# Kernel optimization log

Measured on AMD Instinct MI355X. Metric: run time of the kernel, lower is better.

The kernel has to match this reference:

```python
import jax, jax.numpy as jnp
import numpy as np


def setup_inputs() -> dict:
    key = jax.random.key(0)
    kq, kk, kv, km = jax.random.split(key, 4)
    B, H, S, D = 2, 16, 2048, 64
    Q = jax.random.normal(kq, (B, H, S, D), dtype=jnp.float32)
    K = jax.random.normal(kk, (B, H, S, D), dtype=jnp.float32)
    V = jax.random.normal(kv, (B, H, S, D), dtype=jnp.float32)
    attn_mask = jax.random.randint(km, (B, 1, S, S), 0, 2, dtype=jnp.int32)
    return {"Q": Q, "K": K, "V": V, "attn_mask": attn_mask}


def reference(Q, K, V, attn_mask):
    d_k = jnp.asarray(K.shape[-1], dtype=Q.dtype)
    # scores: [B,H,S,S]
    scores = jnp.einsum("bhqd,bhkd->bhqk", Q, K) / jnp.sqrt(d_k)
    scores = jnp.where(attn_mask == 0, jnp.asarray(-1e9, scores.dtype), scores)
    attn_weights = jax.nn.softmax(scores, axis=-1)
    context = jnp.einsum("bhqk,bhkd->bhqd", attn_weights, V)
    return context, attn_weights
```

## Files before the change

### kernel.cpp

```cpp
#include <hip/hip_runtime.h>
#include <hip/hip_bf16.h>

typedef __attribute__((ext_vector_type(8))) short      short8;
typedef __attribute__((ext_vector_type(4))) float      floatx4;

#define DI __device__ __forceinline__

constexpr int BB = 2, HH = 16, SS = 2048, DD = 64;
constexpr int TQ  = 64;
constexpr int TK  = 64;
constexpr int NKT = SS / TK;
constexpr int PITCH = 72;

DI unsigned short f2bfu(float f) {
    __hip_bfloat16 h = __float2bfloat16(f);
    return __builtin_bit_cast(unsigned short, h);
}

DI short8 cvt8(const float* __restrict__ p) {
    floatx4 a = *(const floatx4*)p;
    floatx4 b = *(const floatx4*)(p + 4);
    short8 r;
    r[0] = (short)f2bfu(a[0]); r[1] = (short)f2bfu(a[1]);
    r[2] = (short)f2bfu(a[2]); r[3] = (short)f2bfu(a[3]);
    r[4] = (short)f2bfu(b[0]); r[5] = (short)f2bfu(b[1]);
    r[6] = (short)f2bfu(b[2]); r[7] = (short)f2bfu(b[3]);
    return r;
}

__global__ __launch_bounds__(256, 2)
void sdpa_kernel(const float* __restrict__ Q,
                 const float* __restrict__ K,
                 const float* __restrict__ V,
                 const int*   __restrict__ mask,
                 float*       __restrict__ out_ctx,
                 float*       __restrict__ out_w)
{
    __shared__ __align__(16) unsigned short Vt[DD * PITCH];
    __shared__ __align__(16) unsigned short Pl[TQ * PITCH];

    const int tid  = (int)threadIdx.x;
    const int wave = tid >> 6;
    const int lane = tid & 63;
    const int quad = lane >> 4;
    const int col  = lane & 15;

    const int bh = (int)blockIdx.y;
    const int b  = bh >> 4;
    const int q0 = (int)blockIdx.x * TQ;
    const int qw = q0 + wave * 16;

    const size_t head = (size_t)bh * SS * DD;
    const float* Qh = Q + head;
    const float* Kh = K + head;
    const float* Vh = V + head;
    const int*   Mb = mask  + (size_t)b  * SS * SS;
    float*       Wh = out_w + (size_t)bh * SS * SS;

    short8 aQ0, aQ1;
    {
        const float* qp = Qh + (size_t)(qw + col) * DD + quad * 8;
        aQ0 = cvt8(qp);
        aQ1 = cvt8(qp + 32);
    }

    float mrow[4], lrow[4];
#pragma unroll
    for (int r = 0; r < 4; ++r) { mrow[r] = -__builtin_inff(); lrow[r] = 0.f; }

    for (int kt = 0; kt < NKT; ++kt) {
        const int kv0 = kt * TK;
        floatx4 acc[4];
#pragma unroll
        for (int nt = 0; nt < 4; ++nt) {
            const float* kp = Kh + (size_t)(kv0 + nt * 16 + col) * DD + quad * 8;
            short8 b0 = cvt8(kp);
            short8 b1 = cvt8(kp + 32);
            floatx4 a = {0.f, 0.f, 0.f, 0.f};
            a = __builtin_amdgcn_mfma_f32_16x16x32_bf16(aQ0, b0, a, 0, 0, 0);
            a = __builtin_amdgcn_mfma_f32_16x16x32_bf16(aQ1, b1, a, 0, 0, 0);
            acc[nt] = a;
        }
#pragma unroll
        for (int r = 0; r < 4; ++r) {
            const int q = qw + quad * 4 + r;
            const int* mp = Mb + (size_t)q * SS + kv0 + col;
            float s0 = acc[0][r] * 0.125f; s0 = (mp[0]  != 0) ? s0 : -1e9f;
            float s1 = acc[1][r] * 0.125f; s1 = (mp[16] != 0) ? s1 : -1e9f;
            float s2 = acc[2][r] * 0.125f; s2 = (mp[32] != 0) ? s2 : -1e9f;
            float s3 = acc[3][r] * 0.125f; s3 = (mp[48] != 0) ? s3 : -1e9f;
            float lm = fmaxf(fmaxf(s0, s1), fmaxf(s2, s3));
            float mn = fmaxf(mrow[r], lm);
            float p  = __expf(s0 - mn) + __expf(s1 - mn) + __expf(s2 - mn) + __expf(s3 - mn);
            lrow[r]  = lrow[r] * __expf(mrow[r] - mn) + p;
            mrow[r]  = mn;
        }
    }
#pragma unroll
    for (int r = 0; r < 4; ++r) {
#pragma unroll
        for (int off = 1; off < 16; off <<= 1) {
            float mo = __shfl_xor(mrow[r], off);
            float lo = __shfl_xor(lrow[r], off);
            float mn = fmaxf(mrow[r], mo);
            lrow[r] = lrow[r] * __expf(mrow[r] - mn) + lo * __expf(mo - mn);
            mrow[r] = mn;
        }
    }
    float rl[4];
#pragma unroll
    for (int r = 0; r < 4; ++r) rl[r] = 1.0f / lrow[r];

    floatx4 ctx[4];
#pragma unroll
    for (int nt = 0; nt < 4; ++nt) ctx[nt] = floatx4{0.f, 0.f, 0.f, 0.f};

    for (int kt = 0; kt < NKT; ++kt) {
        const int kv0 = kt * TK;

        floatx4 acc[4];
#pragma unroll
        for (int nt = 0; nt < 4; ++nt) {
            const float* kp = Kh + (size_t)(kv0 + nt * 16 + col) * DD + quad * 8;
            short8 b0 = cvt8(kp);
            short8 b1 = cvt8(kp + 32);
            floatx4 a = {0.f, 0.f, 0.f, 0.f};
            a = __builtin_amdgcn_mfma_f32_16x16x32_bf16(aQ0, b0, a, 0, 0, 0);
            a = __builtin_amdgcn_mfma_f32_16x16x32_bf16(aQ1, b1, a, 0, 0, 0);
            acc[nt] = a;
        }

        __syncthreads();

        {
            const int kvr = tid >> 2;
            const int d0  = (tid & 3) * 16;
            const float* vp = Vh + (size_t)(kv0 + kvr) * DD + d0;
            floatx4 v0 = *(const floatx4*)vp;
            floatx4 v1 = *(const floatx4*)(vp + 4);
            floatx4 v2 = *(const floatx4*)(vp + 8);
            floatx4 v3 = *(const floatx4*)(vp + 12);
#pragma unroll
            for (int i = 0; i < 4; ++i) Vt[(d0 + i)      * PITCH + kvr] = f2bfu(v0[i]);
#pragma unroll
            for (int i = 0; i < 4; ++i) Vt[(d0 + 4 + i)  * PITCH + kvr] = f2bfu(v1[i]);
#pragma unroll
            for (int i = 0; i < 4; ++i) Vt[(d0 + 8 + i)  * PITCH + kvr] = f2bfu(v2[i]);
#pragma unroll
            for (int i = 0; i < 4; ++i) Vt[(d0 + 12 + i) * PITCH + kvr] = f2bfu(v3[i]);
        }

#pragma unroll
        for (int r = 0; r < 4; ++r) {
            const int q = qw + quad * 4 + r;
            const int* mp = Mb + (size_t)q * SS + kv0 + col;
            float* wp = Wh + (size_t)q * SS + kv0 + col;
#pragma unroll
            for (int nt = 0; nt < 4; ++nt) {
                float v = acc[nt][r] * 0.125f;
                v = (mp[nt * 16] != 0) ? v : -1e9f;
                float w = __expf(v - mrow[r]) * rl[r];
                wp[nt * 16] = w;
                Pl[(wave * 16 + quad * 4 + r) * PITCH + nt * 16 + col] = f2bfu(w);
            }
        }

        __syncthreads();

        short8 pA0 = *(const short8*)&Pl[(wave * 16 + col) * PITCH + quad * 8];
        short8 pA1 = *(const short8*)&Pl[(wave * 16 + col) * PITCH + 32 + quad * 8];
#pragma unroll
        for (int nt = 0; nt < 4; ++nt) {
            short8 vB0 = *(const short8*)&Vt[(nt * 16 + col) * PITCH + quad * 8];
            short8 vB1 = *(const short8*)&Vt[(nt * 16 + col) * PITCH + 32 + quad * 8];
            ctx[nt] = __builtin_amdgcn_mfma_f32_16x16x32_bf16(pA0, vB0, ctx[nt], 0, 0, 0);
            ctx[nt] = __builtin_amdgcn_mfma_f32_16x16x32_bf16(pA1, vB1, ctx[nt], 0, 0, 0);
        }
    }

#pragma unroll
    for (int nt = 0; nt < 4; ++nt) {
#pragma unroll
        for (int r = 0; r < 4; ++r) {
            const int q = qw + quad * 4 + r;
            out_ctx[head + (size_t)q * DD + nt * 16 + col] = ctx[nt][r];
        }
    }
}

extern "C" void kernel_launch(void* const* d_in, const int* in_sizes, int n_in,
                              void* d_out, int out_size, void* d_ws, size_t ws_size,
                              hipStream_t stream) {
    const float* Q = (const float*)d_in[0];
    const float* K = (const float*)d_in[1];
    const float* V = (const float*)d_in[2];
    const int* mask = (const int*)d_in[3];

    float* out     = (float*)d_out;
    float* out_ctx = out;
    float* out_w   = out + (size_t)BB * HH * SS * DD;

    dim3 grid(SS / TQ, BB * HH);
    hipLaunchKernelGGL(sdpa_kernel, grid, dim3(256), 0, stream,
                       Q, K, V, mask, out_ctx, out_w);
}
```

Before: 1.051 ms.

## Precompute bf16 K, transposed V and bitpacked mask in a prep kernel

Adds a prep kernel that converts K to bf16, writes V transposed in bf16 to workspace, and packs the int32 mask into 64-bit ballot words. The main kernel becomes one 64-thread wave per 16 query rows. It reads the preconverted operands directly, folds the 1/sqrt(d) scale into Q, and stages probabilities in LDS so attention weights go out as coalesced nontemporal vector stores. This removes repeated per-block fp32 to bf16 conversion and the heavy int32 mask reads in both passes, at the cost of an extra launch, workspace traffic, and smaller blocks with more global V loads.

New measurement: 889.2 us. 1.18x faster.

```diff
diff --git a/kernel.cpp b/kernel.cpp
--- a/kernel.cpp
+++ b/kernel.cpp
@@ -3,23 +3,27 @@
 
 typedef __attribute__((ext_vector_type(8))) short      short8;
 typedef __attribute__((ext_vector_type(4))) float      floatx4;
+typedef unsigned long long u64;
+typedef unsigned short     u16;
 
 #define DI __device__ __forceinline__
 
 constexpr int BB = 2, HH = 16, SS = 2048, DD = 64;
-constexpr int TQ  = 64;
 constexpr int TK  = 64;
 constexpr int NKT = SS / TK;
-constexpr int PITCH = 72;
-
-DI unsigned short f2bfu(float f) {
+constexpr int PW  = 68;
+
+constexpr size_t NELEM  = (size_t)BB * HH * SS * DD;
+constexpr size_t OFF_VT = NELEM * 2;
+constexpr size_t OFF_MB = OFF_VT + NELEM * 2;
+constexpr size_t NWORDS = (size_t)BB * SS * (SS / 64);
+
+DI u16 f2bfu(float f) {
     __hip_bfloat16 h = __float2bfloat16(f);
-    return __builtin_bit_cast(unsigned short, h);
-}
-
-DI short8 cvt8(const float* __restrict__ p) {
-    floatx4 a = *(const floatx4*)p;
-    floatx4 b = *(const floatx4*)(p + 4);
+    return __builtin_bit_cast(u16, h);
+}
+
+DI short8 pack8(floatx4 a, floatx4 b) {
     short8 r;
     r[0] = (short)f2bfu(a[0]); r[1] = (short)f2bfu(a[1]);
     r[2] = (short)f2bfu(a[2]); r[3] = (short)f2bfu(a[3]);
@@ -28,40 +32,99 @@
     return r;
 }
 
-__global__ __launch_bounds__(256, 2)
-void sdpa_kernel(const float* __restrict__ Q,
-                 const float* __restrict__ K,
-                 const float* __restrict__ V,
-                 const int*   __restrict__ mask,
-                 float*       __restrict__ out_ctx,
-                 float*       __restrict__ out_w)
+DI short8 cvt8s(const float* __restrict__ p, float s) {
+    floatx4 a = *(const floatx4*)p;
+    floatx4 b = *(const floatx4*)(p + 4);
+    a *= s; b *= s;
+    return pack8(a, b);
+}
+
+constexpr int KBLK = 2048;
+constexpr int VBLK = 1024;
+constexpr int MBLK = 4096;
+
+__global__ __launch_bounds__(256)
+void prep_kernel(const float* __restrict__ K, const float* __restrict__ V,
+                 const int* __restrict__ mask,
+                 u16* __restrict__ Kb, u16* __restrict__ Vt, u64* __restrict__ Mb)
 {
-    __shared__ __align__(16) unsigned short Vt[DD * PITCH];
-    __shared__ __align__(16) unsigned short Pl[TQ * PITCH];
-
-    const int tid  = (int)threadIdx.x;
-    const int wave = tid >> 6;
-    const int lane = tid & 63;
+    const int bx = (int)blockIdx.x, tid = (int)threadIdx.x;
+    if (bx < KBLK) {
+        size_t i = ((size_t)bx * 256 + tid) * 8;
+        floatx4 a = *(const floatx4*)(K + i);
+        floatx4 b = *(const floatx4*)(K + i + 4);
+        *(short8*)(Kb + i) = pack8(a, b);
+    } else if (bx < KBLK + VBLK) {
+        __shared__ __align__(16) u16 T[DD * 72];
+        const int idx = bx - KBLK;
+        const int bh = idx >> 5, kt = idx & 31;
+        const int kvr = tid >> 2, d0 = (tid & 3) * 16;
+        const float* vp = V + ((size_t)bh * SS + kt * 64 + kvr) * DD + d0;
+        floatx4 v0 = *(const floatx4*)vp;
+        floatx4 v1 = *(const floatx4*)(vp + 4);
+        floatx4 v2 = *(const floatx4*)(vp + 8);
+        floatx4 v3 = *(const floatx4*)(vp + 12);
+#pragma unroll
+        for (int i = 0; i < 4; ++i) T[(d0 + i)      * 72 + kvr] = f2bfu(v0[i]);
+#pragma unroll
+        for (int i = 0; i < 4; ++i) T[(d0 + 4 + i)  * 72 + kvr] = f2bfu(v1[i]);
+#pragma unroll
+        for (int i = 0; i < 4; ++i) T[(d0 + 8 + i)  * 72 + kvr] = f2bfu(v2[i]);
+#pragma unroll
+        for (int i = 0; i < 4; ++i) T[(d0 + 12 + i) * 72 + kvr] = f2bfu(v3[i]);
+        __syncthreads();
+        const int d = tid >> 2, seg = (tid & 3) * 16;
+        short8 s0 = *(const short8*)&T[d * 72 + seg];
+        short8 s1 = *(const short8*)&T[d * 72 + seg + 8];
+        u16* op = Vt + ((size_t)bh * DD + d) * SS + kt * 64 + seg;
+        *(short8*)op       = s0;
+        *(short8*)(op + 8) = s1;
+    } else {
+        const int mc = bx - (KBLK + VBLK);
+        const int wv = tid >> 6, lane = tid & 63;
+        const size_t gw = (size_t)mc * 4 + wv;
+#pragma unroll
+        for (int it = 0; it < 8; ++it) {
+            size_t word = gw * 8 + it;
+            int b   = (int)(word >> 16);
+            int rem = (int)(word & 65535);
+            int q = rem >> 5, wj = rem & 31;
+            int v = mask[((size_t)b * SS + q) * SS + wj * 64 + lane];
+            u64 bal = __ballot(v != 0);
+            if (lane == 0) Mb[word] = bal;
+        }
+    }
+}
+
+__global__ __launch_bounds__(64, 4)
+void sdpa_main(const float* __restrict__ Q,
+               const u16*   __restrict__ Kb,
+               const u16*   __restrict__ Vt,
+               const u64*   __restrict__ Mb,
+               float*       __restrict__ out_ctx,
+               float*       __restrict__ out_w)
+{
+    __shared__ __align__(16) float Pw[16 * PW];
+
+    const int lane = (int)threadIdx.x;
     const int quad = lane >> 4;
     const int col  = lane & 15;
 
     const int bh = (int)blockIdx.y;
     const int b  = bh >> 4;
-    const int q0 = (int)blockIdx.x * TQ;
-    const int qw = q0 + wave * 16;
+    const int q0 = (int)blockIdx.x * 16;
 
     const size_t head = (size_t)bh * SS * DD;
-    const float* Qh = Q + head;
-    const float* Kh = K + head;
-    const float* Vh = V + head;
-    const int*   Mb = mask  + (size_t)b  * SS * SS;
-    float*       Wh = out_w + (size_t)bh * SS * SS;
+    const u16* Kh = Kb + head;
+    const u16* Vh = Vt + head;
+    const u64* Mh = Mb + ((size_t)b * SS + q0) * (SS / 64);
+    float*     Wh = out_w + (size_t)bh * SS * SS;
 
     short8 aQ0, aQ1;
     {
-        const float* qp = Qh + (size_t)(qw + col) * DD + quad * 8;
-        aQ0 = cvt8(qp);
-        aQ1 = cvt8(qp + 32);
+        const float* qp = Q + head + (size_t)(q0 + col) * DD + quad * 8;
+        aQ0 = cvt8s(qp, 0.125f);
+        aQ1 = cvt8s(qp + 32, 0.125f);
     }
 
     float mrow[4], lrow[4];
@@ -73,9 +136,9 @@
         floatx4 acc[4];
 #pragma unroll
         for (int nt = 0; nt < 4; ++nt) {
-            const float* kp = Kh + (size_t)(kv0 + nt * 16 + col) * DD + quad * 8;
-            short8 b0 = cvt8(kp);
-            short8 b1 = cvt8(kp + 32);
+            const u16* kp = Kh + (size_t)(kv0 + nt * 16 + col) * DD + quad * 8;
+            short8 b0 = *(const short8*)kp;
+            short8 b1 = *(const short8*)(kp + 32);
             floatx4 a = {0.f, 0.f, 0.f, 0.f};
             a = __builtin_amdgcn_mfma_f32_16x16x32_bf16(aQ0, b0, a, 0, 0, 0);
             a = __builtin_amdgcn_mfma_f32_16x16x32_bf16(aQ1, b1, a, 0, 0, 0);
@@ -83,15 +146,17 @@
         }
 #pragma unroll
         for (int r = 0; r < 4; ++r) {
-            const int q = qw + quad * 4 + r;
-            const int* mp = Mb + (size_t)q * SS + kv0 + col;
-            float s0 = acc[0][r] * 0.125f; s0 = (mp[0]  != 0) ? s0 : -1e9f;
-            float s1 = acc[1][r] * 0.125f; s1 = (mp[16] != 0) ? s1 : -1e9f;
-            float s2 = acc[2][r] * 0.125f; s2 = (mp[32] != 0) ? s2 : -1e9f;
-            float s3 = acc[3][r] * 0.125f; s3 = (mp[48] != 0) ? s3 : -1e9f;
-            float lm = fmaxf(fmaxf(s0, s1), fmaxf(s2, s3));
+            const int rloc = quad * 4 + r;
+            const u64 mw = Mh[(size_t)rloc * (SS / 64) + kt];
+            float s[4];
+#pragma unroll
+            for (int nt = 0; nt < 4; ++nt) {
+                unsigned mnt = (unsigned)(mw >> (nt * 16));
+                s[nt] = ((mnt >> col) & 1u) ? acc[nt][r] : -1e9f;
+            }
+            float lm = fmaxf(fmaxf(s[0], s[1]), fmaxf(s[2], s[3]));
             float mn = fmaxf(mrow[r], lm);
-            float p  = __expf(s0 - mn) + __expf(s1 - mn) + __expf(s2 - mn) + __expf(s3 - mn);
+            float p  = __expf(s[0] - mn) + __expf(s[1] - mn) + __expf(s[2] - mn) + __expf(s[3] - mn);
             lrow[r]  = lrow[r] * __expf(mrow[r] - mn) + p;
             mrow[r]  = mn;
         }
@@ -121,69 +186,61 @@
         floatx4 acc[4];
 #pragma unroll
         for (int nt = 0; nt < 4; ++nt) {
-            const float* kp = Kh + (size_t)(kv0 + nt * 16 + col) * DD + quad * 8;
-            short8 b0 = cvt8(kp);
-            short8 b1 = cvt8(kp + 32);
+            const u16* kp = Kh + (size_t)(kv0 + nt * 16 + col) * DD + quad * 8;
+            short8 b0 = *(const short8*)kp;
+            short8 b1 = *(const short8*)(kp + 32);
             floatx4 a = {0.f, 0.f, 0.f, 0.f};
             a = __builtin_amdgcn_mfma_f32_16x16x32_bf16(aQ0, b0, a, 0, 0, 0);
             a = __builtin_amdgcn_mfma_f32_16x16x32_bf16(aQ1, b1, a, 0, 0, 0);
             acc[nt] = a;
         }
 
+#pragma unroll
+        for (int r = 0; r < 4; ++r) {
+            const int rloc = quad * 4 + r;
+            const u64 mw = Mh[(size_t)rloc * (SS / 64) + kt];
+#pragma unroll
+            for (int nt = 0; nt < 4; ++nt) {
+                unsigned mnt = (unsigned)(mw >> (nt * 16));
+                float sv = ((mnt >> col) & 1u) ? acc[nt][r] : -1e9f;
+                Pw[rloc * PW + nt * 16 + col] = __expf(sv - mrow[r]) * rl[r];
+            }
+        }
         __syncthreads();
 
-        {
-            const int kvr = tid >> 2;
-            const int d0  = (tid & 3) * 16;
-            const float* vp = Vh + (size_t)(kv0 + kvr) * DD + d0;
-            floatx4 v0 = *(const floatx4*)vp;
-            floatx4 v1 = *(const floatx4*)(vp + 4);
-            floatx4 v2 = *(const floatx4*)(vp + 8);
-            floatx4 v3 = *(const floatx4*)(vp + 12);
-#pragma unroll
-            for (int i = 0; i < 4; ++i) Vt[(d0 + i)      * PITCH + kvr] = f2bfu(v0[i]);
-#pragma unroll
-            for (int i = 0; i < 4; ++i) Vt[(d0 + 4 + i)  * PITCH + kvr] = f2bfu(v1[i]);
-#pragma unroll
-            for (int i = 0; i < 4; ++i) Vt[(d0 + 8 + i)  * PITCH + kvr] = f2bfu(v2[i]);
-#pragma unroll
-            for (int i = 0; i < 4; ++i) Vt[(d0 + 12 + i) * PITCH + kvr] = f2bfu(v3[i]);
-        }
-
-#pragma unroll
-        for (int r = 0; r < 4; ++r) {
-            const int q = qw + quad * 4 + r;
-            const int* mp = Mb + (size_t)q * SS + kv0 + col;
-            float* wp = Wh + (size_t)q * SS + kv0 + col;
-#pragma unroll
-            for (int nt = 0; nt < 4; ++nt) {
-                float v = acc[nt][r] * 0.125f;
-                v = (mp[nt * 16] != 0) ? v : -1e9f;
-                float w = __expf(v - mrow[r]) * rl[r];
-                wp[nt * 16] = w;
-                Pl[(wave * 16 + quad * 4 + r) * PITCH + nt * 16 + col] = f2bfu(w);
-            }
-        }
-
-        __syncthreads();
-
-        short8 pA0 = *(const short8*)&Pl[(wave * 16 + col) * PITCH + quad * 8];
-        short8 pA1 = *(const short8*)&Pl[(wave * 16 + col) * PITCH + 32 + quad * 8];
+        floatx4 pf0 = *(const floatx4*)&Pw[col * PW + quad * 8];
+        floatx4 pf1 = *(const floatx4*)&Pw[col * PW + quad * 8 + 4];
+        floatx4 pf2 = *(const floatx4*)&Pw[col * PW + 32 + quad * 8];
+        floatx4 pf3 = *(const floatx4*)&Pw[col * PW + 32 + quad * 8 + 4];
+        short8 pA0 = pack8(pf0, pf1);
+        short8 pA1 = pack8(pf2, pf3);
+
+#pragma unroll
+        for (int i = 0; i < 4; ++i) {
+            const int wr = (lane >> 4) + i * 4;
+            const int c4 = (lane & 15) * 4;
+            floatx4 wv = *(const floatx4*)&Pw[wr * PW + c4];
+            __builtin_nontemporal_store(wv, (floatx4*)(Wh + (size_t)(q0 + wr) * SS + kv0 + c4));
+        }
+
 #pragma unroll
         for (int nt = 0; nt < 4; ++nt) {
-            short8 vB0 = *(const short8*)&Vt[(nt * 16 + col) * PITCH + quad * 8];
-            short8 vB1 = *(const short8*)&Vt[(nt * 16 + col) * PITCH + 32 + quad * 8];
+            const u16* vp = Vh + (size_t)(nt * 16 + col) * SS + kv0 + quad * 8;
+            short8 vB0 = *(const short8*)vp;
+            short8 vB1 = *(const short8*)(vp + 32);
             ctx[nt] = __builtin_amdgcn_mfma_f32_16x16x32_bf16(pA0, vB0, ctx[nt], 0, 0, 0);
             ctx[nt] = __builtin_amdgcn_mfma_f32_16x16x32_bf16(pA1, vB1, ctx[nt], 0, 0, 0);
         }
+        __syncthreads();
     }
 
 #pragma unroll
     for (int nt = 0; nt < 4; ++nt) {
 #pragma unroll
         for (int r = 0; r < 4; ++r) {
-            const int q = qw + quad * 4 + r;
-            out_ctx[head + (size_t)q * DD + nt * 16 + col] = ctx[nt][r];
+            const int q = q0 + quad * 4 + r;
+            __builtin_nontemporal_store(ctx[nt][r],
+                out_ctx + head + (size_t)q * DD + nt * 16 + col);
         }
     }
 }
@@ -200,7 +257,13 @@
     float* out_ctx = out;
     float* out_w   = out + (size_t)BB * HH * SS * DD;
 
-    dim3 grid(SS / TQ, BB * HH);
-    hipLaunchKernelGGL(sdpa_kernel, grid, dim3(256), 0, stream,
-                       Q, K, V, mask, out_ctx, out_w);
-}
+    u16* Kb = (u16*)d_ws;
+    u16* Vt = (u16*)((char*)d_ws + OFF_VT);
+    u64* Mb = (u64*)((char*)d_ws + OFF_MB);
+    (void)ws_size;
+
+    hipLaunchKernelGGL(prep_kernel, dim3(KBLK + VBLK + MBLK), dim3(256), 0, stream,
+                       K, V, mask, Kb, Vt, Mb);
+    hipLaunchKernelGGL(sdpa_main, dim3(SS / 16, BB * HH), dim3(64), 0, stream,
+                       Q, Kb, Vt, Mb, out_ctx, out_w);
+}
```
